# Optimization experiments

Measured on AMD Instinct MI355X. Metric: run time of the kernel, lower is better.

Reference implementation:

```python
import jax, jax.numpy as jnp
import numpy as np

C = 1.2            # PoincareBall curvature (learnable in torch, init value used)
SQC = C ** 0.5
MIN_NORM = 1e-15
BALL_EPS = 4e-3    # geoopt float32 projx eps

def _artanh(x):
    return jnp.arctanh(jnp.clip(x, -1.0 + 1e-7, 1.0 - 1e-7))

def _tanh(x):
    return jnp.tanh(jnp.clip(x, -15.0, 15.0))

def _norm(x):
    return jnp.maximum(jnp.linalg.norm(x, axis=-1, keepdims=True), MIN_NORM)

def p_projx(x):
    n = _norm(x)
    maxnorm = (1.0 - BALL_EPS) / SQC
    return jnp.where(n > maxnorm, x / n * maxnorm, x)

def p_expmap0(u):
    n = _norm(u)
    return p_projx(_tanh(SQC * n) * u / (SQC * n))

def p_logmap0(y):
    n = _norm(y)
    return _artanh(SQC * n) * y / (SQC * n)

def p_mobius_add(x, y):
    x2 = jnp.sum(x * x, -1, keepdims=True)
    y2 = jnp.sum(y * y, -1, keepdims=True)
    xy = jnp.sum(x * y, -1, keepdims=True)
    num = (1 + 2 * C * xy + C * y2) * x + (1 - C * x2) * y
    den = 1 + 2 * C * xy + C * C * x2 * y2
    return num / jnp.maximum(den, MIN_NORM)

def p_mobius_matvec(W, x):
    xn = _norm(x)
    mx = x @ W.T
    mxn = _norm(mx)
    res = _tanh(mxn / xn * _artanh(SQC * xn)) * mx / (mxn * SQC)
    zero = jnp.all(mx == 0, axis=-1, keepdims=True)
    return p_projx(jnp.where(zero, jnp.zeros_like(res), res))

def p_mobius_scalar_mul(r, x):
    n = _norm(x)
    return p_projx(_tanh(r * _artanh(SQC * n)) * x / (n * SQC))

def p_linear(x, W, b):
    # Manifold_Linear on PoincareBall: mobius matvec + mobius bias add + projx
    mv = p_mobius_matvec(W, x)
    return p_projx(p_mobius_add(mv, p_expmap0(b)))

def e_linear(x, W, b):
    return x @ W.T + b

def mob_relu(x):
    # Mob_Act: logmap0 -> act -> expmap0 (with projection)
    return p_expmap0(jax.nn.relu(p_logmap0(x)))


def setup_inputs() -> dict:
    key = jax.random.key(0)
    ks = jax.random.split(key, 26)
    g = lambda i, shape, s: (jax.random.normal(ks[i], shape, jnp.float32) * s)
    d = {
        'x':   g(0, (1024, 32, 128), 1.0),
        'We1': g(1, (80, 32), 0.1),   'be1': g(2, (80,), 0.05),
        'We2': g(3, (104, 80), 0.1),  'be2': g(4, (104,), 0.05),
        'We3': g(5, (128, 104), 0.1), 'be3': g(6, (128,), 0.05),
        'Wh1': g(7, (80, 32), 0.1),   'bh1': g(8, (80,), 0.05),
        'Wh2': g(9, (104, 80), 0.1),  'bh2': g(10, (104,), 0.05),
        'Wh3': g(11, (128, 104), 0.1),'bh3': g(12, (128,), 0.05),
        'Wae': g(13, (128, 128), 0.1),'bae': g(14, (128,), 0.05),
        'Wah': g(15, (128, 128), 0.1),'bah': g(16, (128,), 0.05),
        'Wte': g(17, (1, 128), 0.1),  'bte': g(18, (1,), 0.05),
        'Wth': g(19, (1, 128), 0.1),  'bth': g(20, (1,), 0.05),
        'Wf1': g(21, (10, 256), 0.1), 'bf1': g(22, (10,), 0.05),
        'Wf2': g(23, (10, 10), 0.1),  'bf2': g(24, (10,), 0.05),
    }
    return d


def reference(x, We1, be1, We2, be2, We3, be3,
              Wh1, bh1, Wh2, bh2, Wh3, bh3,
              Wae, bae, Wah, bah, Wte, bte, Wth, bth,
              Wf1, bf1, Wf2, bf2):
    xs = jnp.transpose(x, (0, 2, 1))  # (B, S, C_in)

    # --- Euclidean branch: expmap0 = identity; Manifold_Linear = plain linear ---
    xe = xs
    xe = e_linear(xe, We1, be1); xe = jax.nn.relu(xe)
    xe = e_linear(xe, We2, be2); xe = jax.nn.relu(xe)
    xe = e_linear(xe, We3, be3)
    out_e = jax.nn.relu(xe)               # extra self.act for Euclidean manifolds

    # --- Poincare branch ---
    xh = p_expmap0(xs)
    xh = p_linear(xh, Wh1, bh1); xh = mob_relu(xh)
    xh = p_linear(xh, Wh2, bh2); xh = mob_relu(xh)
    out_h = p_linear(xh, Wh3, bh3)        # (B, S, part_dim)

    # --- cross-manifold attention in tangent space at origin ---
    tan_e = e_linear(out_e, Wae, bae)                    # Euclidean logmap0 = id
    tan_h = p_logmap0(p_linear(out_h, Wah, bah))
    mu = 0.5 * (tan_e + tan_h)
    a_e = e_linear(tan_e - mu, Wte, bte)  # (B, S, 1)
    a_h = e_linear(tan_h - mu, Wth, bth)
    w = jax.nn.softmax(jnp.stack([a_e, a_h], axis=0), axis=0)
    proc_e = w[0] * out_e                                # Euclidean mobius scalar mul
    proc_h = p_mobius_scalar_mul(w[1], out_h)

    # --- pool over constituents in tangent space, concat, classify ---
    o_e = jnp.mean(proc_e, axis=1)                       # Euclidean logmap0 = id
    o_h = jnp.mean(p_logmap0(proc_h), axis=1)
    o = jnp.concatenate([o_e, o_h], axis=-1)             # (B, 2*part_dim)
    o = jax.nn.relu(e_linear(o, Wf1, bf1))
    return e_linear(o, Wf2, bf2)
```

## Files before the change

kernel.cpp:

```cpp
#include <hip/hip_runtime.h>
#include <math.h>

constexpr float CC   = 1.2f;
constexpr float SQC  = 1.09544511501033215f;
constexpr float MAXN = (1.0f - 4e-3f) / SQC;
constexpr float MINN = 1e-15f;

constexpr int WTH1 = 0;
constexpr int WTH2 = 4096;
constexpr int WTH3 = 14336;
constexpr int WTAH = 27648;
constexpr int WTE1 = 44032;
constexpr int WTE2 = 48128;
constexpr int WTE3 = 58368;
constexpr int EB1  = 71680;
constexpr int EB2  = 71808;
constexpr int EB3  = 71936;
constexpr int EBA  = 72064;
constexpr int BE1  = 72192;
constexpr int BE2  = 72320;
constexpr int BE3  = 72448;
constexpr int U1o  = 72576;
constexpr int U2o  = 72704;
constexpr int SCo  = 72832;
constexpr int PART = 72864;

constexpr int ASTR  = 65;
constexpr int L_ACT = 0;
constexpr int L_ZH  = 8320;
constexpr int L_SCR = 8960;
constexpr int L_TOT = 9728;

__device__ __forceinline__ float art_(float x){
  x = fminf(fmaxf(x, -0.9999999f), 0.9999999f);
  return 0.5f * __logf((1.0f + x) / (1.0f - x));
}
__device__ __forceinline__ float tanh_(float x){
  x = fminf(fmaxf(x, -15.0f), 15.0f);
  float e = __expf(2.0f * x);
  return (e - 1.0f) / (e + 1.0f);
}
__device__ __forceinline__ float wsum(float v){
#pragma unroll
  for(int i=32;i>0;i>>=1) v += __shfl_xor(v, i, 64);
  return v;
}
__device__ __forceinline__ float rtj(float v){
  v += __shfl_xor(v, 1, 64); v += __shfl_xor(v, 2, 64);
  v += __shfl_xor(v, 4, 64); v += __shfl_xor(v, 8, 64);
  return v;
}
__device__ __forceinline__ float lamv(float nv){
  float n = fmaxf(nv, MINN);
  return art_(SQC*n)/(SQC*n);
}
struct HS { float ca, cb, nv; };
__device__ __forceinline__ HS hyper_chain(float m2, float meb, float xn_in, float y2){
  float xn  = fmaxf(xn_in, MINN);
  float mxn = fmaxf(sqrtf(m2), MINN);
  float r   = art_(SQC*xn);
  float s   = tanh_(mxn/xn*r)/(mxn*SQC);
  float nr  = s*mxn;
  if(nr > MAXN){ s *= MAXN/nr; nr = MAXN; }
  float xy = s*meb, x2 = nr*nr;
  float den = fmaxf(1.f + 2.f*CC*xy + CC*CC*x2*y2, MINN);
  float A   = (1.f + 2.f*CC*xy + CC*y2)/den;
  float Bc  = (1.f - CC*x2)/den;
  float n3  = sqrtf(fmaxf(A*A*x2 + 2.f*A*Bc*xy + Bc*Bc*y2, 0.f));
  float rho = (n3 > MAXN) ? MAXN/n3 : 1.f;
  HS h; h.nv = fminf(n3, MAXN); h.ca = rho*A*s; h.cb = rho*Bc;
  return h;
}
struct TT { float tau, nf; };
__device__ __forceinline__ TT tail_relu(float rn2){
  float rn = fmaxf(sqrtf(rn2), MINN);
  float th = tanh_(SQC*rn);
  TT r; r.tau = th/(SQC*rn); r.nf = th/SQC;
  if(r.nf > MAXN){ r.tau *= MAXN/r.nf; r.nf = MAXN; }
  return r;
}
struct EX { float nh, scl; };
__device__ __forceinline__ EX exp0(float n2){
  float n0 = fmaxf(sqrtf(n2), MINN);
  float th = tanh_(SQC*n0);
  EX e; e.nh = th/SQC; e.scl = th/(SQC*n0);
  if(e.nh > MAXN){ e.scl *= MAXN/e.nh; e.nh = MAXN; }
  return e;
}
struct THW { float te, th2; };
__device__ __forceinline__ THW ahchain(float m2a, float mw1, float mw2, float meba,
                                       float xnh, float rr, float y2,
                                       float ebw1, float ebw2){
  float mxn = fmaxf(sqrtf(m2a), MINN);
  float s = tanh_(mxn/xnh*rr)/(mxn*SQC);
  float nr = s*mxn;
  if(nr > MAXN){ s *= MAXN/nr; nr = MAXN; }
  float xy = s*meba, x2 = nr*nr;
  float den = fmaxf(1.f + 2.f*CC*xy + CC*CC*x2*y2, MINN);
  float A = (1.f + 2.f*CC*xy + CC*y2)/den;
  float Bc = (1.f - CC*x2)/den;
  float n3 = sqrtf(fmaxf(A*A*x2 + 2.f*A*Bc*xy + Bc*Bc*y2, 0.f));
  float rho = (n3 > MAXN) ? MAXN/n3 : 1.f;
  float nv = fminf(n3, MAXN);
  float lr = lamv(nv)*rho;
  THW r; r.te = lr*(A*s*mw1 + Bc*ebw1); r.th2 = lr*(A*s*mw2 + Bc*ebw2);
  return r;
}
struct AG { float wge, g2; };
__device__ __forceinline__ AG attn(float d1, float d2, float thte, float thth,
                                   float rr, float xnh, float b_e, float b_h){
  float a_e = 0.5f*(d1 - thte) + b_e;
  float a_h = 0.5f*(thth - d2) + b_h;
  float mx = fmaxf(a_e, a_h);
  float ee = __expf(a_e - mx), eh = __expf(a_h - mx);
  float inv = 1.f/(ee + eh);
  AG r; r.wge = ee*inv;
  float wgh = eh*inv;
  float inner = wgh*rr;
  float scl2 = tanh_(inner)/(xnh*SQC);
  float nn = scl2*xnh;
  if(nn > MAXN){ scl2 *= MAXN/nn; nn = MAXN; }
  r.g2 = lamv(nn)*scl2;
  return r;
}

__global__ void k_setup_a(const float* __restrict__ Wae, const float* __restrict__ bae,
                          const float* __restrict__ bh1, const float* __restrict__ bh2,
                          const float* __restrict__ bh3, const float* __restrict__ bah,
                          const float* __restrict__ Wte, const float* __restrict__ Wth,
                          const float* __restrict__ be1, const float* __restrict__ be2,
                          const float* __restrict__ be3, float* __restrict__ ws){
  const int tid = threadIdx.x;
  {
    const int which = tid >> 7, k = tid & 127;
    const float* wv = which ? Wth : Wte;
    float s = 0.f;
#pragma unroll 4
    for(int j=0;j<128;++j) s += Wae[j*128+k] * wv[j];
    ws[(which ? U2o : U1o) + k] = s;
  }
  if(tid < 128){
    ws[BE1+tid] = (tid < 80)  ? be1[tid] : 0.f;
    ws[BE2+tid] = (tid < 104) ? be2[tid] : 0.f;
    ws[BE3+tid] = be3[tid];
  }
  if(tid < 64){
    const int l = tid;
    float p1=0.f, p2=0.f;
    for(int j=l;j<128;j+=64){ p1 += bae[j]*Wte[j]; p2 += bae[j]*Wth[j]; }
    p1 = wsum(p1); p2 = wsum(p2);
    if(l==0){ ws[SCo+0]=p1; ws[SCo+1]=p2; }
    const float* bs[4] = {bh1,bh2,bh3,bah};
    const int dims[4]  = {80,104,128,128};
    const int offs[4]  = {EB1,EB2,EB3,EBA};
    for(int v=0;v<4;++v){
      const float* bp = bs[v]; const int D = dims[v];
      float q = 0.f;
      for(int j=l;j<D;j+=64) q += bp[j]*bp[j];
      q = wsum(q);
      float nb = fmaxf(sqrtf(q), MINN);
      float th = tanhf(fminf(fmaxf(SQC*nb,-15.f),15.f));
      float coef = th/(SQC*nb);
      float ne = th/SQC;
      if(ne > MAXN){ coef *= MAXN/ne; ne = MAXN; }
      for(int j=l;j<D;j+=64) ws[offs[v]+j] = coef*bp[j];
      for(int j=D+l;j<128;j+=64) ws[offs[v]+j] = 0.f;
      if(l==0) ws[SCo+2+v] = ne*ne;
      if(v==3){
        float e1=0.f, e2=0.f;
        for(int j=l;j<D;j+=64){ e1 += bp[j]*Wte[j]; e2 += bp[j]*Wth[j]; }
        e1 = wsum(e1)*coef; e2 = wsum(e2)*coef;
        if(l==0){ ws[SCo+6]=e1; ws[SCo+7]=e2; }
      }
    }
  }
}

__global__ void k_trans(const float* __restrict__ Wh1, const float* __restrict__ Wh2,
                        const float* __restrict__ Wh3, const float* __restrict__ Wah,
                        const float* __restrict__ We1, const float* __restrict__ We2,
                        const float* __restrict__ We3, float* __restrict__ ws){
  const int blk = blockIdx.x, j = threadIdx.x;
  const float* W; int OUT, K, kk, dst;
  if(blk < 32)       { W=Wh1; OUT=80;  K=32;  kk=blk;      dst=WTH1; }
  else if(blk < 112) { W=Wh2; OUT=104; K=80;  kk=blk-32;   dst=WTH2; }
  else if(blk < 216) { W=Wh3; OUT=128; K=104; kk=blk-112;  dst=WTH3; }
  else if(blk < 344) { W=Wah; OUT=128; K=128; kk=blk-216;  dst=WTAH; }
  else if(blk < 376) { W=We1; OUT=80;  K=32;  kk=blk-344;  dst=WTE1; }
  else if(blk < 456) { W=We2; OUT=104; K=80;  kk=blk-376;  dst=WTE2; }
  else               { W=We3; OUT=128; K=104; kk=blk-456;  dst=WTE3; }
  ws[dst + kk*128 + j] = (j < OUT) ? W[j*K + kk] : 0.f;
}

__global__ void k_fin(const float* __restrict__ ws, const float* __restrict__ bf1,
                      const float* __restrict__ Wf2, const float* __restrict__ bf2,
                      float* __restrict__ out){
  const int r = blockIdx.x*64 + threadIdx.x;
  const float* p = ws + PART + (size_t)r*20;
  float f1[10];
#pragma unroll
  for(int i=0;i<10;++i)
    f1[i] = fmaxf((p[i] + p[10+i])*(1.f/128.f) + bf1[i], 0.f);
#pragma unroll
  for(int o=0;o<10;++o){
    float a = bf2[o];
#pragma unroll
    for(int k=0;k<10;++k) a = fmaf(Wf2[o*10+k], f1[k], a);
    out[r*10 + o] = a;
  }
}

__device__ __forceinline__ void ld8(const float* __restrict__ p, float (&v)[8]){
  float4 a = *(const float4*)p, b = *(const float4*)(p+4);
  v[0]=a.x; v[1]=a.y; v[2]=a.z; v[3]=a.w; v[4]=b.x; v[5]=b.y; v[6]=b.z; v[7]=b.w;
}

template<int K, bool XG, bool XSQ>
__device__ __forceinline__ void gemm4(const float* __restrict__ wt,
                                      const float* __restrict__ xg,
                                      const float* __restrict__ ACT,
                                      int tj, int tt, float (&acc)[4][8], float (&xsq)[4]){
#pragma unroll
  for(int i=0;i<4;++i)
#pragma unroll
    for(int j=0;j<8;++j) acc[i][j] = 0.f;
  const int wo = tj*8, xo = tt*4;
#pragma unroll 4
  for(int k=0;k<K;++k){
    float4 w0 = *(const float4*)(wt + k*128 + wo);
    float4 w1 = *(const float4*)(wt + k*128 + wo + 4);
    float4 xa;
    if(XG) xa = *(const float4*)(xg + k*128 + xo);
    else   xa = *(const float4*)(ACT + k*ASTR + xo);
    float xv[4] = {xa.x,xa.y,xa.z,xa.w};
    float wv[8] = {w0.x,w0.y,w0.z,w0.w,w1.x,w1.y,w1.z,w1.w};
#pragma unroll
    for(int i=0;i<4;++i){
      if(XSQ) xsq[i] = fmaf(xv[i], xv[i], xsq[i]);
#pragma unroll
      for(int j=0;j<8;++j) acc[i][j] = fmaf(xv[i], wv[j], acc[i][j]);
    }
  }
}

__device__ __forceinline__ void wACT(float* __restrict__ ACT, const float (&acc)[4][8],
                                     int tj, int tt){
#pragma unroll
  for(int j=0;j<8;++j){
    float4 a = {acc[0][j],acc[1][j],acc[2][j],acc[3][j]};
    *(float4*)(ACT + (tj*8+j)*ASTR + tt*4) = a;
  }
}

__global__ __launch_bounds__(256, 4) void k_main(
    const float* __restrict__ x,
    const float* __restrict__ Wf1, const float* __restrict__ Wte,
    const float* __restrict__ bte, const float* __restrict__ Wth,
    const float* __restrict__ bth, float* __restrict__ ws){
  extern __shared__ float lds[];
  float* ACT = lds + L_ACT;
  float* ZH  = lds + L_ZH;
  float* SCR = lds + L_SCR;
  const int tid = threadIdx.x, tj = tid & 15, tt = tid >> 4;
  const int b = blockIdx.x, b2 = b >> 1, hf = b & 1;
  const int tok0 = tt*4;
  const bool isTok = tid < 64;
  const float* xg = x + (size_t)b2*4096 + hf*64;

  float acc[4][8];
  float xsq[4];
#pragma unroll
  for(int i=0;i<4;++i) xsq[i] = 0.f;

  float nf = 0.f, rr = 0.f, xnh = 1.f, thte = 0.f, thth = 0.f;

  {
    gemm4<32,true,true>(ws+WTH1, xg, ACT, tj, tt, acc, xsq);
    float ebv[8]; ld8(ws+EB1+tj*8, ebv);
#pragma unroll
    for(int i=0;i<4;++i){
      float s=0.f, e=0.f;
#pragma unroll
      for(int j=0;j<8;++j){ s = fmaf(acc[i][j],acc[i][j],s); e = fmaf(acc[i][j],ebv[j],e); }
      s = rtj(s); e = rtj(e);
      if(tj==0){ SCR[tok0+i]=s; SCR[64+tok0+i]=e; SCR[128+tok0+i]=xsq[i]; }
    }
    __syncthreads();
    if(isTok){
      EX e0 = exp0(SCR[128+tid]);
      float scl0 = e0.scl;
      float m2 = SCR[tid]*scl0*scl0, meb = SCR[64+tid]*scl0;
      HS h = hyper_chain(m2, meb, e0.nh, ws[SCo+2]);
      SCR[tid] = h.ca*scl0; SCR[64+tid] = h.cb; SCR[128+tid] = lamv(h.nv);
    }
    __syncthreads();
    float cav[4],cbv[4],lmv[4];
#pragma unroll
    for(int i=0;i<4;++i){ cav[i]=SCR[tok0+i]; cbv[i]=SCR[64+tok0+i]; lmv[i]=SCR[128+tok0+i]; }
#pragma unroll
    for(int i=0;i<4;++i){
      float s=0.f;
#pragma unroll
      for(int j=0;j<8;++j){
        float v = fmaxf(lmv[i]*fmaf(cav[i],acc[i][j],cbv[i]*ebv[j]), 0.f);
        acc[i][j]=v; s = fmaf(v,v,s);
      }
      s = rtj(s);
      if(tj==0) SCR[192+tok0+i]=s;
    }
    __syncthreads();
    if(isTok){ TT tr = tail_relu(SCR[192+tid]); nf = tr.nf; SCR[192+tid]=tr.tau; }
    __syncthreads();
#pragma unroll
    for(int i=0;i<4;++i){ float tau=SCR[192+tok0+i];
#pragma unroll
      for(int j=0;j<8;++j) acc[i][j]*=tau; }
    wACT(ACT, acc, tj, tt);
    __syncthreads();
  }

  {
    gemm4<80,false,false>(ws+WTH2, nullptr, ACT, tj, tt, acc, xsq);
    float ebv[8]; ld8(ws+EB2+tj*8, ebv);
#pragma unroll
    for(int i=0;i<4;++i){
      float s=0.f, e=0.f;
#pragma unroll
      for(int j=0;j<8;++j){ s = fmaf(acc[i][j],acc[i][j],s); e = fmaf(acc[i][j],ebv[j],e); }
      s = rtj(s); e = rtj(e);
      if(tj==0){ SCR[tok0+i]=s; SCR[64+tok0+i]=e; }
    }
    __syncthreads();
    if(isTok){
      HS h = hyper_chain(SCR[tid], SCR[64+tid], nf, ws[SCo+3]);
      SCR[tid]=h.ca; SCR[64+tid]=h.cb; SCR[128+tid]=lamv(h.nv);
    }
    __syncthreads();
    float cav[4],cbv[4],lmv[4];
#pragma unroll
    for(int i=0;i<4;++i){ cav[i]=SCR[tok0+i]; cbv[i]=SCR[64+tok0+i]; lmv[i]=SCR[128+tok0+i]; }
#pragma unroll
    for(int i=0;i<4;++i){
      float s=0.f;
#pragma unroll
      for(int j=0;j<8;++j){
        float v = fmaxf(lmv[i]*fmaf(cav[i],acc[i][j],cbv[i]*ebv[j]), 0.f);
        acc[i][j]=v; s = fmaf(v,v,s);
      }
      s = rtj(s);
      if(tj==0) SCR[192+tok0+i]=s;
    }
    __syncthreads();
    if(isTok){ TT tr = tail_relu(SCR[192+tid]); nf = tr.nf; SCR[192+tid]=tr.tau; }
    __syncthreads();
#pragma unroll
    for(int i=0;i<4;++i){ float tau=SCR[192+tok0+i];
#pragma unroll
      for(int j=0;j<8;++j) acc[i][j]*=tau; }
    wACT(ACT, acc, tj, tt);
    __syncthreads();
  }

  {
    gemm4<104,false,false>(ws+WTH3, nullptr, ACT, tj, tt, acc, xsq);
    float ebv[8]; ld8(ws+EB3+tj*8, ebv);
#pragma unroll
    for(int i=0;i<4;++i){
      float s=0.f, e=0.f;
#pragma unroll
      for(int j=0;j<8;++j){ s = fmaf(acc[i][j],acc[i][j],s); e = fmaf(acc[i][j],ebv[j],e); }
      s = rtj(s); e = rtj(e);
      if(tj==0){ SCR[tok0+i]=s; SCR[64+tok0+i]=e; }
    }
    __syncthreads();
    if(isTok){
      HS h = hyper_chain(SCR[tid], SCR[64+tid], nf, ws[SCo+4]);
      xnh = fmaxf(h.nv, MINN);
      rr  = art_(SQC*xnh);
      SCR[tid]=h.ca; SCR[64+tid]=h.cb;
    }
    __syncthreads();
    float cav[4],cbv[4];
#pragma unroll
    for(int i=0;i<4;++i){ cav[i]=SCR[tok0+i]; cbv[i]=SCR[64+tok0+i]; }
#pragma unroll
    for(int i=0;i<4;++i)
#pragma unroll
      for(int j=0;j<8;++j) acc[i][j] = fmaf(cav[i],acc[i][j],cbv[i]*ebv[j]);
    wACT(ACT, acc, tj, tt);
#pragma unroll
    for(int ic=0;ic<10;++ic){
      float wf[8]; ld8(Wf1 + ic*256 + 128 + tj*8, wf);
#pragma unroll
      for(int i=0;i<4;++i){
        float s=0.f;
#pragma unroll
        for(int j=0;j<8;++j) s = fmaf(acc[i][j], wf[j], s);
        s = rtj(s);
        if(tj==0) ZH[ic*64 + tok0 + i] = s;
      }
    }
    __syncthreads();
  }

  {
    gemm4<128,false,false>(ws+WTAH, nullptr, ACT, tj, tt, acc, xsq);
    float w1v[8], w2v[8], eav[8];
    ld8(Wte + tj*8, w1v); ld8(Wth + tj*8, w2v); ld8(ws+EBA+tj*8, eav);
#pragma unroll
    for(int i=0;i<4;++i){
      float s0=0.f,s1=0.f,s2=0.f,s3=0.f;
#pragma unroll
      for(int j=0;j<8;++j){
        float m = acc[i][j];
        s0 = fmaf(m,m,s0); s1 = fmaf(m,w1v[j],s1);
        s2 = fmaf(m,w2v[j],s2); s3 = fmaf(m,eav[j],s3);
      }
      s0=rtj(s0); s1=rtj(s1); s2=rtj(s2); s3=rtj(s3);
      if(tj==0){ SCR[tok0+i]=s0; SCR[64+tok0+i]=s1; SCR[128+tok0+i]=s2; SCR[192+tok0+i]=s3; }
    }
    __syncthreads();
    if(isTok){
      THW a = ahchain(SCR[tid], SCR[64+tid], SCR[128+tid], SCR[192+tid],
                      xnh, rr, ws[SCo+5], ws[SCo+6], ws[SCo+7]);
      thte = a.te; thth = a.th2;
    }
  }

  {
    gemm4<32,true,false>(ws+WTE1, xg, ACT, tj, tt, acc, xsq);
    float bev[8]; ld8(ws+BE1+tj*8, bev);
#pragma unroll
    for(int i=0;i<4;++i)
#pragma unroll
      for(int j=0;j<8;++j) acc[i][j] = fmaxf(acc[i][j]+bev[j], 0.f);
    __syncthreads();
    wACT(ACT, acc, tj, tt);
    __syncthreads();
  }
  {
    gemm4<80,false,false>(ws+WTE2, nullptr, ACT, tj, tt, acc, xsq);
    float bev[8]; ld8(ws+BE2+tj*8, bev);
#pragma unroll
    for(int i=0;i<4;++i)
#pragma unroll
      for(int j=0;j<8;++j) acc[i][j] = fmaxf(acc[i][j]+bev[j], 0.f);
    __syncthreads();
    wACT(ACT, acc, tj, tt);
    __syncthreads();
  }
  {
    gemm4<104,false,false>(ws+WTE3, nullptr, ACT, tj, tt, acc, xsq);
    float bev[8], u1v[8], u2v[8];
    ld8(ws+BE3+tj*8, bev); ld8(ws+U1o+tj*8, u1v); ld8(ws+U2o+tj*8, u2v);
#pragma unroll
    for(int i=0;i<4;++i){
      float s1=0.f, s2=0.f;
#pragma unroll
      for(int j=0;j<8;++j){
        float v = fmaxf(acc[i][j]+bev[j], 0.f);
        acc[i][j] = v;
        s1 = fmaf(v,u1v[j],s1); s2 = fmaf(v,u2v[j],s2);
      }
      s1=rtj(s1); s2=rtj(s2);
      if(tj==0){ SCR[tok0+i]=s1; SCR[64+tok0+i]=s2; }
    }
#pragma unroll
    for(int ic=0;ic<10;++ic){
      float wf[8]; ld8(Wf1 + ic*256 + tj*8, wf);
#pragma unroll
      for(int i=0;i<4;++i){
        float s=0.f;
#pragma unroll
        for(int j=0;j<8;++j) s = fmaf(acc[i][j], wf[j], s);
        s = rtj(s);
        if(tj==0) SCR[(2+ic)*64 + tok0 + i] = s;
      }
    }
    __syncthreads();
    if(isTok){
      float d1 = SCR[tid] + ws[SCo+0];
      float d2 = SCR[64+tid] + ws[SCo+1];
      AG g = attn(d1, d2, thte, thth, rr, xnh, bte[0], bth[0]);
      float pv[10];
#pragma unroll
      for(int ic=0;ic<10;++ic){
        float p = fmaf(g.wge, SCR[(2+ic)*64+tid], g.g2 * ZH[ic*64+tid]);
        pv[ic] = wsum(p);
      }
      if(tid == 0){
#pragma unroll
        for(int ic=0;ic<10;++ic) ws[PART + (size_t)b*10 + ic] = pv[ic];
      }
    }
  }
}

extern "C" void kernel_launch(void* const* d_in, const int* in_sizes, int n_in,
                              void* d_out, int out_size, void* d_ws, size_t ws_size,
                              hipStream_t stream){
  (void)in_sizes; (void)n_in; (void)out_size; (void)ws_size;
  const float* x   = (const float*)d_in[0];
  const float* We1 = (const float*)d_in[1];
  const float* be1 = (const float*)d_in[2];
  const float* We2 = (const float*)d_in[3];
  const float* be2 = (const float*)d_in[4];
  const float* We3 = (const float*)d_in[5];
  const float* be3 = (const float*)d_in[6];
  const float* Wh1 = (const float*)d_in[7];
  const float* bh1 = (const float*)d_in[8];
  const float* Wh2 = (const float*)d_in[9];
  const float* bh2 = (const float*)d_in[10];
  const float* Wh3 = (const float*)d_in[11];
  const float* bh3 = (const float*)d_in[12];
  const float* Wae = (const float*)d_in[13];
  const float* bae = (const float*)d_in[14];
  const float* Wah = (const float*)d_in[15];
  const float* bah = (const float*)d_in[16];
  const float* Wte = (const float*)d_in[17];
  const float* bte = (const float*)d_in[18];
  const float* Wth = (const float*)d_in[19];
  const float* bth = (const float*)d_in[20];
  const float* Wf1 = (const float*)d_in[21];
  const float* bf1 = (const float*)d_in[22];
  const float* Wf2 = (const float*)d_in[23];
  const float* bf2 = (const float*)d_in[24];
  float* ws  = (float*)d_ws;
  float* out = (float*)d_out;

  hipLaunchKernelGGL(k_setup_a, dim3(1), dim3(256), 0, stream,
                     Wae, bae, bh1, bh2, bh3, bah, Wte, Wth, be1, be2, be3, ws);
  hipLaunchKernelGGL(k_trans, dim3(560), dim3(128), 0, stream,
                     Wh1, Wh2, Wh3, Wah, We1, We2, We3, ws);

  const int smem = L_TOT * 4;
  hipLaunchKernelGGL(k_main, dim3(2048), dim3(256), smem, stream,
                     x, Wf1, Wte, bte, Wth, bth, ws);

  hipLaunchKernelGGL(k_fin, dim3(16), dim3(64), 0, stream,
                     ws, bf1, Wf2, bf2, out);
}
```

Baseline: 568.6 us.

## Compute per-token hyperbolic scalars redundantly in every lane, removing block barriers

Per-token scalar chains (hyper_chain, tail_relu, ahchain, attn) were computed by 64 threads through LDS staging with several __syncthreads per layer. They are now computed redundantly in each of the 16 lanes that hold a token, right after the row reductions, so most barriers and LDS round-trips go away. The final pooling reduces with shuffles plus a small cross-wave LDS sum, and the setup and transpose kernels are merged into one launch. LDS allocation shrinks, which may help occupancy. In exchange, all lanes repeat the transcendental math and register pressure rises from the per-token arrays.

```diff
diff --git a/kernel.cpp b/kernel.cpp
--- a/kernel.cpp
+++ b/kernel.cpp
@@ -29,7 +29,7 @@
 constexpr int L_ACT = 0;
 constexpr int L_ZH  = 8320;
 constexpr int L_SCR = 8960;
-constexpr int L_TOT = 9728;
+constexpr int L_TOT = 9000;
 
 __device__ __forceinline__ float art_(float x){
   x = fminf(fmaxf(x, -0.9999999f), 0.9999999f);
@@ -124,13 +124,31 @@
   return r;
 }
 
-__global__ void k_setup_a(const float* __restrict__ Wae, const float* __restrict__ bae,
-                          const float* __restrict__ bh1, const float* __restrict__ bh2,
-                          const float* __restrict__ bh3, const float* __restrict__ bah,
-                          const float* __restrict__ Wte, const float* __restrict__ Wth,
-                          const float* __restrict__ be1, const float* __restrict__ be2,
-                          const float* __restrict__ be3, float* __restrict__ ws){
-  const int tid = threadIdx.x;
+__global__ void k_setup(const float* __restrict__ Wh1, const float* __restrict__ Wh2,
+                        const float* __restrict__ Wh3, const float* __restrict__ Wah,
+                        const float* __restrict__ We1, const float* __restrict__ We2,
+                        const float* __restrict__ We3,
+                        const float* __restrict__ Wae, const float* __restrict__ bae,
+                        const float* __restrict__ bh1, const float* __restrict__ bh2,
+                        const float* __restrict__ bh3, const float* __restrict__ bah,
+                        const float* __restrict__ Wte, const float* __restrict__ Wth,
+                        const float* __restrict__ be1, const float* __restrict__ be2,
+                        const float* __restrict__ be3, float* __restrict__ ws){
+  const int blk = blockIdx.x, tid = threadIdx.x;
+  if(blk < 280){
+    const int row = blk*2 + (tid >> 7);
+    const int j   = tid & 127;
+    const float* W; int OUT, K, kk, dst;
+    if(row < 32)       { W=Wh1; OUT=80;  K=32;  kk=row;      dst=WTH1; }
+    else if(row < 112) { W=Wh2; OUT=104; K=80;  kk=row-32;   dst=WTH2; }
+    else if(row < 216) { W=Wh3; OUT=128; K=104; kk=row-112;  dst=WTH3; }
+    else if(row < 344) { W=Wah; OUT=128; K=128; kk=row-216;  dst=WTAH; }
+    else if(row < 376) { W=We1; OUT=80;  K=32;  kk=row-344;  dst=WTE1; }
+    else if(row < 456) { W=We2; OUT=104; K=80;  kk=row-376;  dst=WTE2; }
+    else               { W=We3; OUT=128; K=104; kk=row-456;  dst=WTE3; }
+    ws[dst + kk*128 + j] = (j < OUT) ? W[j*K + kk] : 0.f;
+    return;
+  }
   {
     const int which = tid >> 7, k = tid & 127;
     const float* wv = which ? Wth : Wte;
@@ -176,22 +194,6 @@
   }
 }
 
-__global__ void k_trans(const float* __restrict__ Wh1, const float* __restrict__ Wh2,
-                        const float* __restrict__ Wh3, const float* __restrict__ Wah,
-                        const float* __restrict__ We1, const float* __restrict__ We2,
-                        const float* __restrict__ We3, float* __restrict__ ws){
-  const int blk = blockIdx.x, j = threadIdx.x;
-  const float* W; int OUT, K, kk, dst;
-  if(blk < 32)       { W=Wh1; OUT=80;  K=32;  kk=blk;      dst=WTH1; }
-  else if(blk < 112) { W=Wh2; OUT=104; K=80;  kk=blk-32;   dst=WTH2; }
-  else if(blk < 216) { W=Wh3; OUT=128; K=104; kk=blk-112;  dst=WTH3; }
-  else if(blk < 344) { W=Wah; OUT=128; K=128; kk=blk-216;  dst=WTAH; }
-  else if(blk < 376) { W=We1; OUT=80;  K=32;  kk=blk-344;  dst=WTE1; }
-  else if(blk < 456) { W=We2; OUT=104; K=80;  kk=blk-376;  dst=WTE2; }
-  else               { W=We3; OUT=128; K=104; kk=blk-456;  dst=WTE3; }
-  ws[dst + kk*128 + j] = (j < OUT) ? W[j*K + kk] : 0.f;
-}
-
 __global__ void k_fin(const float* __restrict__ ws, const float* __restrict__ bf1,
                       const float* __restrict__ Wf2, const float* __restrict__ bf2,
                       float* __restrict__ out){
@@ -264,15 +266,19 @@
   const int tid = threadIdx.x, tj = tid & 15, tt = tid >> 4;
   const int b = blockIdx.x, b2 = b >> 1, hf = b & 1;
   const int tok0 = tt*4;
-  const bool isTok = tid < 64;
   const float* xg = x + (size_t)b2*4096 + hf*64;
+
+  const float c1  = ws[SCo+0], c2  = ws[SCo+1];
+  const float y21 = ws[SCo+2], y22 = ws[SCo+3], y23 = ws[SCo+4], y2a = ws[SCo+5];
+  const float ew1 = ws[SCo+6], ew2 = ws[SCo+7];
+  const float btev = bte[0], bthv = bth[0];
 
   float acc[4][8];
   float xsq[4];
 #pragma unroll
   for(int i=0;i<4;++i) xsq[i] = 0.f;
 
-  float nf = 0.f, rr = 0.f, xnh = 1.f, thte = 0.f, thth = 0.f;
+  float nf[4], xnh[4], rr[4], tte[4], tth[4];
 
   {
     gemm4<32,true,true>(ws+WTH1, xg, ACT, tj, tt, acc, xsq);
@@ -283,38 +289,20 @@
 #pragma unroll
       for(int j=0;j<8;++j){ s = fmaf(acc[i][j],acc[i][j],s); e = fmaf(acc[i][j],ebv[j],e); }
       s = rtj(s); e = rtj(e);
-      if(tj==0){ SCR[tok0+i]=s; SCR[64+tok0+i]=e; SCR[128+tok0+i]=xsq[i]; }
-    }
-    __syncthreads();
-    if(isTok){
-      EX e0 = exp0(SCR[128+tid]);
-      float scl0 = e0.scl;
-      float m2 = SCR[tid]*scl0*scl0, meb = SCR[64+tid]*scl0;
-      HS h = hyper_chain(m2, meb, e0.nh, ws[SCo+2]);
-      SCR[tid] = h.ca*scl0; SCR[64+tid] = h.cb; SCR[128+tid] = lamv(h.nv);
-    }
-    __syncthreads();
-    float cav[4],cbv[4],lmv[4];
-#pragma unroll
-    for(int i=0;i<4;++i){ cav[i]=SCR[tok0+i]; cbv[i]=SCR[64+tok0+i]; lmv[i]=SCR[128+tok0+i]; }
-#pragma unroll
-    for(int i=0;i<4;++i){
-      float s=0.f;
+      EX e0 = exp0(xsq[i]);
+      HS h = hyper_chain(s*e0.scl*e0.scl, e*e0.scl, e0.nh, y21);
+      float lam = lamv(h.nv), ca = h.ca*e0.scl, cb = h.cb;
+      float s2 = 0.f;
 #pragma unroll
       for(int j=0;j<8;++j){
-        float v = fmaxf(lmv[i]*fmaf(cav[i],acc[i][j],cbv[i]*ebv[j]), 0.f);
-        acc[i][j]=v; s = fmaf(v,v,s);
-      }
-      s = rtj(s);
-      if(tj==0) SCR[192+tok0+i]=s;
-    }
-    __syncthreads();
-    if(isTok){ TT tr = tail_relu(SCR[192+tid]); nf = tr.nf; SCR[192+tid]=tr.tau; }
-    __syncthreads();
-#pragma unroll
-    for(int i=0;i<4;++i){ float tau=SCR[192+tok0+i];
-#pragma unroll
-      for(int j=0;j<8;++j) acc[i][j]*=tau; }
+        float v = fmaxf(lam*fmaf(ca, acc[i][j], cb*ebv[j]), 0.f);
+        acc[i][j] = v; s2 = fmaf(v,v,s2);
+      }
+      s2 = rtj(s2);
+      TT tr = tail_relu(s2); nf[i] = tr.nf;
+#pragma unroll
+      for(int j=0;j<8;++j) acc[i][j] *= tr.tau;
+    }
     wACT(ACT, acc, tj, tt);
     __syncthreads();
   }
@@ -328,35 +316,20 @@
 #pragma unroll
       for(int j=0;j<8;++j){ s = fmaf(acc[i][j],acc[i][j],s); e = fmaf(acc[i][j],ebv[j],e); }
       s = rtj(s); e = rtj(e);
-      if(tj==0){ SCR[tok0+i]=s; SCR[64+tok0+i]=e; }
-    }
-    __syncthreads();
-    if(isTok){
-      HS h = hyper_chain(SCR[tid], SCR[64+tid], nf, ws[SCo+3]);
-      SCR[tid]=h.ca; SCR[64+tid]=h.cb; SCR[128+tid]=lamv(h.nv);
-    }
-    __syncthreads();
-    float cav[4],cbv[4],lmv[4];
-#pragma unroll
-    for(int i=0;i<4;++i){ cav[i]=SCR[tok0+i]; cbv[i]=SCR[64+tok0+i]; lmv[i]=SCR[128+tok0+i]; }
-#pragma unroll
-    for(int i=0;i<4;++i){
-      float s=0.f;
+      HS h = hyper_chain(s, e, nf[i], y22);
+      float lam = lamv(h.nv);
+      float s2 = 0.f;
 #pragma unroll
       for(int j=0;j<8;++j){
-        float v = fmaxf(lmv[i]*fmaf(cav[i],acc[i][j],cbv[i]*ebv[j]), 0.f);
-        acc[i][j]=v; s = fmaf(v,v,s);
-      }
-      s = rtj(s);
-      if(tj==0) SCR[192+tok0+i]=s;
-    }
-    __syncthreads();
-    if(isTok){ TT tr = tail_relu(SCR[192+tid]); nf = tr.nf; SCR[192+tid]=tr.tau; }
-    __syncthreads();
-#pragma unroll
-    for(int i=0;i<4;++i){ float tau=SCR[192+tok0+i];
-#pragma unroll
-      for(int j=0;j<8;++j) acc[i][j]*=tau; }
+        float v = fmaxf(lam*fmaf(h.ca, acc[i][j], h.cb*ebv[j]), 0.f);
+        acc[i][j] = v; s2 = fmaf(v,v,s2);
+      }
+      s2 = rtj(s2);
+      TT tr = tail_relu(s2); nf[i] = tr.nf;
+#pragma unroll
+      for(int j=0;j<8;++j) acc[i][j] *= tr.tau;
+    }
+    __syncthreads();
     wACT(ACT, acc, tj, tt);
     __syncthreads();
   }
@@ -370,23 +343,13 @@
 #pragma unroll
       for(int j=0;j<8;++j){ s = fmaf(acc[i][j],acc[i][j],s); e = fmaf(acc[i][j],ebv[j],e); }
       s = rtj(s); e = rtj(e);
-      if(tj==0){ SCR[tok0+i]=s; SCR[64+tok0+i]=e; }
-    }
-    __syncthreads();
-    if(isTok){
-      HS h = hyper_chain(SCR[tid], SCR[64+tid], nf, ws[SCo+4]);
-      xnh = fmaxf(h.nv, MINN);
-      rr  = art_(SQC*xnh);
-      SCR[tid]=h.ca; SCR[64+tid]=h.cb;
-    }
-    __syncthreads();
-    float cav[4],cbv[4];
-#pragma unroll
-    for(int i=0;i<4;++i){ cav[i]=SCR[tok0+i]; cbv[i]=SCR[64+tok0+i]; }
-#pragma unroll
-    for(int i=0;i<4;++i)
-#pragma unroll
-      for(int j=0;j<8;++j) acc[i][j] = fmaf(cav[i],acc[i][j],cbv[i]*ebv[j]);
+      HS h = hyper_chain(s, e, nf[i], y23);
+      xnh[i] = fmaxf(h.nv, MINN);
+      rr[i]  = art_(SQC*xnh[i]);
+#pragma unroll
+      for(int j=0;j<8;++j) acc[i][j] = fmaf(h.ca, acc[i][j], h.cb*ebv[j]);
+    }
+    __syncthreads();
     wACT(ACT, acc, tj, tt);
 #pragma unroll
     for(int ic=0;ic<10;++ic){
@@ -417,13 +380,8 @@
         s2 = fmaf(m,w2v[j],s2); s3 = fmaf(m,eav[j],s3);
       }
       s0=rtj(s0); s1=rtj(s1); s2=rtj(s2); s3=rtj(s3);
-      if(tj==0){ SCR[tok0+i]=s0; SCR[64+tok0+i]=s1; SCR[128+tok0+i]=s2; SCR[192+tok0+i]=s3; }
-    }
-    __syncthreads();
-    if(isTok){
-      THW a = ahchain(SCR[tid], SCR[64+tid], SCR[128+tid], SCR[192+tid],
-                      xnh, rr, ws[SCo+5], ws[SCo+6], ws[SCo+7]);
-      thte = a.te; thth = a.th2;
+      THW a = ahchain(s0, s1, s2, s3, xnh[i], rr[i], y2a, ew1, ew2);
+      tte[i] = a.te; tth[i] = a.th2;
     }
   }
 
@@ -453,6 +411,7 @@
     gemm4<104,false,false>(ws+WTE3, nullptr, ACT, tj, tt, acc, xsq);
     float bev[8], u1v[8], u2v[8];
     ld8(ws+BE3+tj*8, bev); ld8(ws+U1o+tj*8, u1v); ld8(ws+U2o+tj*8, u2v);
+    float wge[4], g2v[4];
 #pragma unroll
     for(int i=0;i<4;++i){
       float s1=0.f, s2=0.f;
@@ -462,37 +421,30 @@
         acc[i][j] = v;
         s1 = fmaf(v,u1v[j],s1); s2 = fmaf(v,u2v[j],s2);
       }
-      s1=rtj(s1); s2=rtj(s2);
-      if(tj==0){ SCR[tok0+i]=s1; SCR[64+tok0+i]=s2; }
+      s1 = rtj(s1); s2 = rtj(s2);
+      AG g = attn(s1 + c1, s2 + c2, tte[i], tth[i], rr[i], xnh[i], btev, bthv);
+      wge[i] = g.wge; g2v[i] = g.g2;
     }
 #pragma unroll
     for(int ic=0;ic<10;++ic){
       float wf[8]; ld8(Wf1 + ic*256 + tj*8, wf);
+      float pv = 0.f;
 #pragma unroll
       for(int i=0;i<4;++i){
-        float s=0.f;
-#pragma unroll
-        for(int j=0;j<8;++j) s = fmaf(acc[i][j], wf[j], s);
-        s = rtj(s);
-        if(tj==0) SCR[(2+ic)*64 + tok0 + i] = s;
-      }
-    }
-    __syncthreads();
-    if(isTok){
-      float d1 = SCR[tid] + ws[SCo+0];
-      float d2 = SCR[64+tid] + ws[SCo+1];
-      AG g = attn(d1, d2, thte, thth, rr, xnh, bte[0], bth[0]);
-      float pv[10];
-#pragma unroll
-      for(int ic=0;ic<10;++ic){
-        float p = fmaf(g.wge, SCR[(2+ic)*64+tid], g.g2 * ZH[ic*64+tid]);
-        pv[ic] = wsum(p);
-      }
-      if(tid == 0){
-#pragma unroll
-        for(int ic=0;ic<10;++ic) ws[PART + (size_t)b*10 + ic] = pv[ic];
-      }
-    }
+        float z=0.f;
+#pragma unroll
+        for(int j=0;j<8;++j) z = fmaf(acc[i][j], wf[j], z);
+        z = rtj(z);
+        pv += wge[i]*z + g2v[i]*ZH[ic*64 + tok0 + i];
+      }
+      pv += __shfl_xor(pv, 16, 64);
+      pv += __shfl_xor(pv, 32, 64);
+      if((tid & 63) == 0) SCR[(tid>>6)*10 + ic] = pv;
+    }
+    __syncthreads();
+    if(tid < 10)
+      ws[PART + (size_t)b*10 + tid] =
+        SCR[tid] + SCR[10+tid] + SCR[20+tid] + SCR[30+tid];
   }
 }
 
@@ -528,10 +480,9 @@
   float* ws  = (float*)d_ws;
   float* out = (float*)d_out;
 
-  hipLaunchKernelGGL(k_setup_a, dim3(1), dim3(256), 0, stream,
+  hipLaunchKernelGGL(k_setup, dim3(281), dim3(256), 0, stream,
+                     Wh1, Wh2, Wh3, Wah, We1, We2, We3,
                      Wae, bae, bh1, bh2, bh3, bah, Wte, Wth, be1, be2, be3, ws);
-  hipLaunchKernelGGL(k_trans, dim3(560), dim3(128), 0, stream,
-                     Wh1, Wh2, Wh3, Wah, We1, We2, We3, ws);
 
   const int smem = L_TOT * 4;
   hipLaunchKernelGGL(k_main, dim3(2048), dim3(256), smem, stream,
```

Result: slower. 590.8 us (+3.9%).

## Split each sample across four blocks of 32 tokens and merge setup kernels

Applied to the files above, without the earlier changes.

The main kernel now processes 32 tokens per block instead of 64. The grid doubles to 4096 blocks, the register tile shrinks to 2x8, LDS use drops by about half, and launch bounds rise to 6 blocks per CU to raise occupancy. The final kernel now sums four partials per sample instead of two. The weight-transpose and setup kernels are fused into one launch, and extra barriers are added before the activation writes. In exchange each block reloads the full weights for half as many tokens, so weight traffic per token rises and arithmetic reuse drops.

```diff
diff --git a/kernel.cpp b/kernel.cpp
--- a/kernel.cpp
+++ b/kernel.cpp
@@ -25,11 +25,11 @@
 constexpr int SCo  = 72832;
 constexpr int PART = 72864;
 
-constexpr int ASTR  = 65;
+constexpr int ASTR  = 33;
 constexpr int L_ACT = 0;
-constexpr int L_ZH  = 8320;
-constexpr int L_SCR = 8960;
-constexpr int L_TOT = 9728;
+constexpr int L_ZH  = 4224;
+constexpr int L_SCR = 4544;
+constexpr int L_TOT = 4928;
 
 __device__ __forceinline__ float art_(float x){
   x = fminf(fmaxf(x, -0.9999999f), 0.9999999f);
@@ -48,6 +48,12 @@
 __device__ __forceinline__ float rtj(float v){
   v += __shfl_xor(v, 1, 64); v += __shfl_xor(v, 2, 64);
   v += __shfl_xor(v, 4, 64); v += __shfl_xor(v, 8, 64);
+  return v;
+}
+__device__ __forceinline__ float rt32(float v){
+  v += __shfl_xor(v, 1, 64); v += __shfl_xor(v, 2, 64);
+  v += __shfl_xor(v, 4, 64); v += __shfl_xor(v, 8, 64);
+  v += __shfl_xor(v, 16, 64);
   return v;
 }
 __device__ __forceinline__ float lamv(float nv){
@@ -124,13 +130,31 @@
   return r;
 }
 
-__global__ void k_setup_a(const float* __restrict__ Wae, const float* __restrict__ bae,
-                          const float* __restrict__ bh1, const float* __restrict__ bh2,
-                          const float* __restrict__ bh3, const float* __restrict__ bah,
-                          const float* __restrict__ Wte, const float* __restrict__ Wth,
-                          const float* __restrict__ be1, const float* __restrict__ be2,
-                          const float* __restrict__ be3, float* __restrict__ ws){
-  const int tid = threadIdx.x;
+__global__ void k_setup(const float* __restrict__ Wh1, const float* __restrict__ Wh2,
+                        const float* __restrict__ Wh3, const float* __restrict__ Wah,
+                        const float* __restrict__ We1, const float* __restrict__ We2,
+                        const float* __restrict__ We3,
+                        const float* __restrict__ Wae, const float* __restrict__ bae,
+                        const float* __restrict__ bh1, const float* __restrict__ bh2,
+                        const float* __restrict__ bh3, const float* __restrict__ bah,
+                        const float* __restrict__ Wte, const float* __restrict__ Wth,
+                        const float* __restrict__ be1, const float* __restrict__ be2,
+                        const float* __restrict__ be3, float* __restrict__ ws){
+  const int blk = blockIdx.x, tid = threadIdx.x;
+  if(blk < 280){
+    const int row = blk*2 + (tid >> 7);
+    const int j   = tid & 127;
+    const float* W; int OUT, K, kk, dst;
+    if(row < 32)       { W=Wh1; OUT=80;  K=32;  kk=row;      dst=WTH1; }
+    else if(row < 112) { W=Wh2; OUT=104; K=80;  kk=row-32;   dst=WTH2; }
+    else if(row < 216) { W=Wh3; OUT=128; K=104; kk=row-112;  dst=WTH3; }
+    else if(row < 344) { W=Wah; OUT=128; K=128; kk=row-216;  dst=WTAH; }
+    else if(row < 376) { W=We1; OUT=80;  K=32;  kk=row-344;  dst=WTE1; }
+    else if(row < 456) { W=We2; OUT=104; K=80;  kk=row-376;  dst=WTE2; }
+    else               { W=We3; OUT=128; K=104; kk=row-456;  dst=WTE3; }
+    ws[dst + kk*128 + j] = (j < OUT) ? W[j*K + kk] : 0.f;
+    return;
+  }
   {
     const int which = tid >> 7, k = tid & 127;
     const float* wv = which ? Wth : Wte;
@@ -176,31 +200,15 @@
   }
 }
 
-__global__ void k_trans(const float* __restrict__ Wh1, const float* __restrict__ Wh2,
-                        const float* __restrict__ Wh3, const float* __restrict__ Wah,
-                        const float* __restrict__ We1, const float* __restrict__ We2,
-                        const float* __restrict__ We3, float* __restrict__ ws){
-  const int blk = blockIdx.x, j = threadIdx.x;
-  const float* W; int OUT, K, kk, dst;
-  if(blk < 32)       { W=Wh1; OUT=80;  K=32;  kk=blk;      dst=WTH1; }
-  else if(blk < 112) { W=Wh2; OUT=104; K=80;  kk=blk-32;   dst=WTH2; }
-  else if(blk < 216) { W=Wh3; OUT=128; K=104; kk=blk-112;  dst=WTH3; }
-  else if(blk < 344) { W=Wah; OUT=128; K=128; kk=blk-216;  dst=WTAH; }
-  else if(blk < 376) { W=We1; OUT=80;  K=32;  kk=blk-344;  dst=WTE1; }
-  else if(blk < 456) { W=We2; OUT=104; K=80;  kk=blk-376;  dst=WTE2; }
-  else               { W=We3; OUT=128; K=104; kk=blk-456;  dst=WTE3; }
-  ws[dst + kk*128 + j] = (j < OUT) ? W[j*K + kk] : 0.f;
-}
-
 __global__ void k_fin(const float* __restrict__ ws, const float* __restrict__ bf1,
                       const float* __restrict__ Wf2, const float* __restrict__ bf2,
                       float* __restrict__ out){
   const int r = blockIdx.x*64 + threadIdx.x;
-  const float* p = ws + PART + (size_t)r*20;
+  const float* p = ws + PART + (size_t)r*40;
   float f1[10];
 #pragma unroll
   for(int i=0;i<10;++i)
-    f1[i] = fmaxf((p[i] + p[10+i])*(1.f/128.f) + bf1[i], 0.f);
+    f1[i] = fmaxf((p[i] + p[10+i] + p[20+i] + p[30+i])*(1.f/128.f) + bf1[i], 0.f);
 #pragma unroll
   for(int o=0;o<10;++o){
     float a = bf2[o];
@@ -216,26 +224,26 @@
 }
 
 template<int K, bool XG, bool XSQ>
-__device__ __forceinline__ void gemm4(const float* __restrict__ wt,
+__device__ __forceinline__ void gemm2(const float* __restrict__ wt,
                                       const float* __restrict__ xg,
                                       const float* __restrict__ ACT,
-                                      int tj, int tt, float (&acc)[4][8], float (&xsq)[4]){
-#pragma unroll
-  for(int i=0;i<4;++i)
+                                      int tj, int tt, float (&acc)[2][8], float (&xsq)[2]){
+#pragma unroll
+  for(int i=0;i<2;++i)
 #pragma unroll
     for(int j=0;j<8;++j) acc[i][j] = 0.f;
-  const int wo = tj*8, xo = tt*4;
+  const int wo = tj*8, xo = tt*2;
 #pragma unroll 4
   for(int k=0;k<K;++k){
     float4 w0 = *(const float4*)(wt + k*128 + wo);
     float4 w1 = *(const float4*)(wt + k*128 + wo + 4);
-    float4 xa;
-    if(XG) xa = *(const float4*)(xg + k*128 + xo);
-    else   xa = *(const float4*)(ACT + k*ASTR + xo);
-    float xv[4] = {xa.x,xa.y,xa.z,xa.w};
+    float2 xa;
+    if(XG) xa = *(const float2*)(xg + k*128 + xo);
+    else   xa = *(const float2*)(ACT + k*ASTR + xo);
+    float xv[2] = {xa.x,xa.y};
     float wv[8] = {w0.x,w0.y,w0.z,w0.w,w1.x,w1.y,w1.z,w1.w};
 #pragma unroll
-    for(int i=0;i<4;++i){
+    for(int i=0;i<2;++i){
       if(XSQ) xsq[i] = fmaf(xv[i], xv[i], xsq[i]);
 #pragma unroll
       for(int j=0;j<8;++j) acc[i][j] = fmaf(xv[i], wv[j], acc[i][j]);
@@ -243,16 +251,16 @@
   }
 }
 
-__device__ __forceinline__ void wACT(float* __restrict__ ACT, const float (&acc)[4][8],
+__device__ __forceinline__ void wACT(float* __restrict__ ACT, const float (&acc)[2][8],
                                      int tj, int tt){
 #pragma unroll
   for(int j=0;j<8;++j){
-    float4 a = {acc[0][j],acc[1][j],acc[2][j],acc[3][j]};
-    *(float4*)(ACT + (tj*8+j)*ASTR + tt*4) = a;
-  }
-}
-
-__global__ __launch_bounds__(256, 4) void k_main(
+    float2 a = {acc[0][j],acc[1][j]};
+    *(float2*)(ACT + (tj*8+j)*ASTR + tt*2) = a;
+  }
+}
+
+__global__ __launch_bounds__(256, 6) void k_main(
     const float* __restrict__ x,
     const float* __restrict__ Wf1, const float* __restrict__ Wte,
     const float* __restrict__ bte, const float* __restrict__ Wth,
@@ -262,43 +270,43 @@
   float* ZH  = lds + L_ZH;
   float* SCR = lds + L_SCR;
   const int tid = threadIdx.x, tj = tid & 15, tt = tid >> 4;
-  const int b = blockIdx.x, b2 = b >> 1, hf = b & 1;
-  const int tok0 = tt*4;
-  const bool isTok = tid < 64;
-  const float* xg = x + (size_t)b2*4096 + hf*64;
-
-  float acc[4][8];
-  float xsq[4];
-#pragma unroll
-  for(int i=0;i<4;++i) xsq[i] = 0.f;
+  const int b = blockIdx.x, b2 = b >> 2, q = b & 3;
+  const int tok0 = tt*2;
+  const bool isTok = tid < 32;
+  const float* xg = x + (size_t)b2*4096 + q*32;
+
+  float acc[2][8];
+  float xsq[2];
+#pragma unroll
+  for(int i=0;i<2;++i) xsq[i] = 0.f;
 
   float nf = 0.f, rr = 0.f, xnh = 1.f, thte = 0.f, thth = 0.f;
 
   {
-    gemm4<32,true,true>(ws+WTH1, xg, ACT, tj, tt, acc, xsq);
+    gemm2<32,true,true>(ws+WTH1, xg, ACT, tj, tt, acc, xsq);
     float ebv[8]; ld8(ws+EB1+tj*8, ebv);
 #pragma unroll
-    for(int i=0;i<4;++i){
+    for(int i=0;i<2;++i){
       float s=0.f, e=0.f;
 #pragma unroll
       for(int j=0;j<8;++j){ s = fmaf(acc[i][j],acc[i][j],s); e = fmaf(acc[i][j],ebv[j],e); }
       s = rtj(s); e = rtj(e);
-      if(tj==0){ SCR[tok0+i]=s; SCR[64+tok0+i]=e; SCR[128+tok0+i]=xsq[i]; }
+      if(tj==0){ SCR[tok0+i]=s; SCR[32+tok0+i]=e; SCR[64+tok0+i]=xsq[i]; }
     }
     __syncthreads();
     if(isTok){
-      EX e0 = exp0(SCR[128+tid]);
+      EX e0 = exp0(SCR[64+tid]);
       float scl0 = e0.scl;
-      float m2 = SCR[tid]*scl0*scl0, meb = SCR[64+tid]*scl0;
+      float m2 = SCR[tid]*scl0*scl0, meb = SCR[32+tid]*scl0;
       HS h = hyper_chain(m2, meb, e0.nh, ws[SCo+2]);
-      SCR[tid] = h.ca*scl0; SCR[64+tid] = h.cb; SCR[128+tid] = lamv(h.nv);
-    }
-    __syncthreads();
-    float cav[4],cbv[4],lmv[4];
-#pragma unroll
-    for(int i=0;i<4;++i){ cav[i]=SCR[tok0+i]; cbv[i]=SCR[64+tok0+i]; lmv[i]=SCR[128+tok0+i]; }
-#pragma unroll
-    for(int i=0;i<4;++i){
+      SCR[tid] = h.ca*scl0; SCR[32+tid] = h.cb; SCR[64+tid] = lamv(h.nv);
+    }
+    __syncthreads();
+    float cav[2],cbv[2],lmv[2];
+#pragma unroll
+    for(int i=0;i<2;++i){ cav[i]=SCR[tok0+i]; cbv[i]=SCR[32+tok0+i]; lmv[i]=SCR[64+tok0+i]; }
+#pragma unroll
+    for(int i=0;i<2;++i){
       float s=0.f;
 #pragma unroll
       for(int j=0;j<8;++j){
@@ -306,13 +314,13 @@
         acc[i][j]=v; s = fmaf(v,v,s);
       }
       s = rtj(s);
-      if(tj==0) SCR[192+tok0+i]=s;
-    }
-    __syncthreads();
-    if(isTok){ TT tr = tail_relu(SCR[192+tid]); nf = tr.nf; SCR[192+tid]=tr.tau; }
-    __syncthreads();
-#pragma unroll
-    for(int i=0;i<4;++i){ float tau=SCR[192+tok0+i];
+      if(tj==0) SCR[96+tok0+i]=s;
+    }
+    __syncthreads();
+    if(isTok){ TT tr = tail_relu(SCR[96+tid]); nf = tr.nf; SCR[96+tid]=tr.tau; }
+    __syncthreads();
+#pragma unroll
+    for(int i=0;i<2;++i){ float tau=SCR[96+tok0+i];
 #pragma unroll
       for(int j=0;j<8;++j) acc[i][j]*=tau; }
     wACT(ACT, acc, tj, tt);
@@ -320,27 +328,27 @@
   }
 
   {
-    gemm4<80,false,false>(ws+WTH2, nullptr, ACT, tj, tt, acc, xsq);
+    gemm2<80,false,false>(ws+WTH2, nullptr, ACT, tj, tt, acc, xsq);
     float ebv[8]; ld8(ws+EB2+tj*8, ebv);
 #pragma unroll
-    for(int i=0;i<4;++i){
+    for(int i=0;i<2;++i){
       float s=0.f, e=0.f;
 #pragma unroll
       for(int j=0;j<8;++j){ s = fmaf(acc[i][j],acc[i][j],s); e = fmaf(acc[i][j],ebv[j],e); }
       s = rtj(s); e = rtj(e);
-      if(tj==0){ SCR[tok0+i]=s; SCR[64+tok0+i]=e; }
+      if(tj==0){ SCR[tok0+i]=s; SCR[32+tok0+i]=e; }
     }
     __syncthreads();
     if(isTok){
-      HS h = hyper_chain(SCR[tid], SCR[64+tid], nf, ws[SCo+3]);
-      SCR[tid]=h.ca; SCR[64+tid]=h.cb; SCR[128+tid]=lamv(h.nv);
-    }
-    __syncthreads();
-    float cav[4],cbv[4],lmv[4];
-#pragma unroll
-    for(int i=0;i<4;++i){ cav[i]=SCR[tok0+i]; cbv[i]=SCR[64+tok0+i]; lmv[i]=SCR[128+tok0+i]; }
-#pragma unroll
-    for(int i=0;i<4;++i){
+      HS h = hyper_chain(SCR[tid], SCR[32+tid], nf, ws[SCo+3]);
+      SCR[tid]=h.ca; SCR[32+tid]=h.cb; SCR[64+tid]=lamv(h.nv);
+    }
+    __syncthreads();
+    float cav[2],cbv[2],lmv[2];
+#pragma unroll
+    for(int i=0;i<2;++i){ cav[i]=SCR[tok0+i]; cbv[i]=SCR[32+tok0+i]; lmv[i]=SCR[64+tok0+i]; }
+#pragma unroll
+    for(int i=0;i<2;++i){
       float s=0.f;
 #pragma unroll
       for(int j=0;j<8;++j){
@@ -348,67 +356,69 @@
         acc[i][j]=v; s = fmaf(v,v,s);
       }
       s = rtj(s);
-      if(tj==0) SCR[192+tok0+i]=s;
-    }
-    __syncthreads();
-    if(isTok){ TT tr = tail_relu(SCR[192+tid]); nf = tr.nf; SCR[192+tid]=tr.tau; }
-    __syncthreads();
-#pragma unroll
-    for(int i=0;i<4;++i){ float tau=SCR[192+tok0+i];
+      if(tj==0) SCR[96+tok0+i]=s;
+    }
+    __syncthreads();
+    if(isTok){ TT tr = tail_relu(SCR[96+tid]); nf = tr.nf; SCR[96+tid]=tr.tau; }
+    __syncthreads();
+#pragma unroll
+    for(int i=0;i<2;++i){ float tau=SCR[96+tok0+i];
 #pragma unroll
       for(int j=0;j<8;++j) acc[i][j]*=tau; }
+    __syncthreads();
     wACT(ACT, acc, tj, tt);
     __syncthreads();
   }
 
   {
-    gemm4<104,false,false>(ws+WTH3, nullptr, ACT, tj, tt, acc, xsq);
+    gemm2<104,false,false>(ws+WTH3, nullptr, ACT, tj, tt, acc, xsq);
     float ebv[8]; ld8(ws+EB3+tj*8, ebv);
 #pragma unroll
-    for(int i=0;i<4;++i){
+    for(int i=0;i<2;++i){
       float s=0.f, e=0.f;
 #pragma unroll
       for(int j=0;j<8;++j){ s = fmaf(acc[i][j],acc[i][j],s); e = fmaf(acc[i][j],ebv[j],e); }
       s = rtj(s); e = rtj(e);
-      if(tj==0){ SCR[tok0+i]=s; SCR[64+tok0+i]=e; }
+      if(tj==0){ SCR[tok0+i]=s; SCR[32+tok0+i]=e; }
     }
     __syncthreads();
     if(isTok){
-      HS h = hyper_chain(SCR[tid], SCR[64+tid], nf, ws[SCo+4]);
+      HS h = hyper_chain(SCR[tid], SCR[32+tid], nf, ws[SCo+4]);
       xnh = fmaxf(h.nv, MINN);
       rr  = art_(SQC*xnh);
-      SCR[tid]=h.ca; SCR[64+tid]=h.cb;
-    }
-    __syncthreads();
-    float cav[4],cbv[4];
-#pragma unroll
-    for(int i=0;i<4;++i){ cav[i]=SCR[tok0+i]; cbv[i]=SCR[64+tok0+i]; }
-#pragma unroll
-    for(int i=0;i<4;++i)
+      SCR[tid]=h.ca; SCR[32+tid]=h.cb;
+    }
+    __syncthreads();
+    float cav[2],cbv[2];
+#pragma unroll
+    for(int i=0;i<2;++i){ cav[i]=SCR[tok0+i]; cbv[i]=SCR[32+tok0+i]; }
+#pragma unroll
+    for(int i=0;i<2;++i)
 #pragma unroll
       for(int j=0;j<8;++j) acc[i][j] = fmaf(cav[i],acc[i][j],cbv[i]*ebv[j]);
+    __syncthreads();
     wACT(ACT, acc, tj, tt);
 #pragma unroll
     for(int ic=0;ic<10;++ic){
       float wf[8]; ld8(Wf1 + ic*256 + 128 + tj*8, wf);
 #pragma unroll
-      for(int i=0;i<4;++i){
+      for(int i=0;i<2;++i){
         float s=0.f;
 #pragma unroll
         for(int j=0;j<8;++j) s = fmaf(acc[i][j], wf[j], s);
         s = rtj(s);
-        if(tj==0) ZH[ic*64 + tok0 + i] = s;
-      }
-    }
-    __syncthreads();
-  }
-
-  {
-    gemm4<128,false,false>(ws+WTAH, nullptr, ACT, tj, tt, acc, xsq);
+        if(tj==0) ZH[ic*32 + tok0 + i] = s;
+      }
+    }
+    __syncthreads();
+  }
+
+  {
+    gemm2<128,false,false>(ws+WTAH, nullptr, ACT, tj, tt, acc, xsq);
     float w1v[8], w2v[8], eav[8];
     ld8(Wte + tj*8, w1v); ld8(Wth + tj*8, w2v); ld8(ws+EBA+tj*8, eav);
 #pragma unroll
-    for(int i=0;i<4;++i){
+    for(int i=0;i<2;++i){
       float s0=0.f,s1=0.f,s2=0.f,s3=0.f;
 #pragma unroll
       for(int j=0;j<8;++j){
@@ -417,21 +427,21 @@
         s2 = fmaf(m,w2v[j],s2); s3 = fmaf(m,eav[j],s3);
       }
       s0=rtj(s0); s1=rtj(s1); s2=rtj(s2); s3=rtj(s3);
-      if(tj==0){ SCR[tok0+i]=s0; SCR[64+tok0+i]=s1; SCR[128+tok0+i]=s2; SCR[192+tok0+i]=s3; }
+      if(tj==0){ SCR[tok0+i]=s0; SCR[32+tok0+i]=s1; SCR[64+tok0+i]=s2; SCR[96+tok0+i]=s3; }
     }
     __syncthreads();
     if(isTok){
-      THW a = ahchain(SCR[tid], SCR[64+tid], SCR[128+tid], SCR[192+tid],
+      THW a = ahchain(SCR[tid], SCR[32+tid], SCR[64+tid], SCR[96+tid],
                       xnh, rr, ws[SCo+5], ws[SCo+6], ws[SCo+7]);
       thte = a.te; thth = a.th2;
     }
   }
 
   {
-    gemm4<32,true,false>(ws+WTE1, xg, ACT, tj, tt, acc, xsq);
+    gemm2<32,true,false>(ws+WTE1, xg, ACT, tj, tt, acc, xsq);
     float bev[8]; ld8(ws+BE1+tj*8, bev);
 #pragma unroll
-    for(int i=0;i<4;++i)
+    for(int i=0;i<2;++i)
 #pragma unroll
       for(int j=0;j<8;++j) acc[i][j] = fmaxf(acc[i][j]+bev[j], 0.f);
     __syncthreads();
@@ -439,10 +449,10 @@
     __syncthreads();
   }
   {
-    gemm4<80,false,false>(ws+WTE2, nullptr, ACT, tj, tt, acc, xsq);
+    gemm2<80,false,false>(ws+WTE2, nullptr, ACT, tj, tt, acc, xsq);
     float bev[8]; ld8(ws+BE2+tj*8, bev);
 #pragma unroll
-    for(int i=0;i<4;++i)
+    for(int i=0;i<2;++i)
 #pragma unroll
       for(int j=0;j<8;++j) acc[i][j] = fmaxf(acc[i][j]+bev[j], 0.f);
     __syncthreads();
@@ -450,11 +460,11 @@
     __syncthreads();
   }
   {
-    gemm4<104,false,false>(ws+WTE3, nullptr, ACT, tj, tt, acc, xsq);
+    gemm2<104,false,false>(ws+WTE3, nullptr, ACT, tj, tt, acc, xsq);
     float bev[8], u1v[8], u2v[8];
     ld8(ws+BE3+tj*8, bev); ld8(ws+U1o+tj*8, u1v); ld8(ws+U2o+tj*8, u2v);
 #pragma unroll
-    for(int i=0;i<4;++i){
+    for(int i=0;i<2;++i){
       float s1=0.f, s2=0.f;
 #pragma unroll
       for(int j=0;j<8;++j){
@@ -463,30 +473,30 @@
         s1 = fmaf(v,u1v[j],s1); s2 = fmaf(v,u2v[j],s2);
       }
       s1=rtj(s1); s2=rtj(s2);
-      if(tj==0){ SCR[tok0+i]=s1; SCR[64+tok0+i]=s2; }
+      if(tj==0){ SCR[tok0+i]=s1; SCR[32+tok0+i]=s2; }
     }
 #pragma unroll
     for(int ic=0;ic<10;++ic){
       float wf[8]; ld8(Wf1 + ic*256 + tj*8, wf);
 #pragma unroll
-      for(int i=0;i<4;++i){
+      for(int i=0;i<2;++i){
         float s=0.f;
 #pragma unroll
         for(int j=0;j<8;++j) s = fmaf(acc[i][j], wf[j], s);
         s = rtj(s);
-        if(tj==0) SCR[(2+ic)*64 + tok0 + i] = s;
+        if(tj==0) SCR[(2+ic)*32 + tok0 + i] = s;
       }
     }
     __syncthreads();
     if(isTok){
       float d1 = SCR[tid] + ws[SCo+0];
-      float d2 = SCR[64+tid] + ws[SCo+1];
+      float d2 = SCR[32+tid] + ws[SCo+1];
       AG g = attn(d1, d2, thte, thth, rr, xnh, bte[0], bth[0]);
       float pv[10];
 #pragma unroll
       for(int ic=0;ic<10;++ic){
-        float p = fmaf(g.wge, SCR[(2+ic)*64+tid], g.g2 * ZH[ic*64+tid]);
-        pv[ic] = wsum(p);
+        float p = fmaf(g.wge, SCR[(2+ic)*32+tid], g.g2 * ZH[ic*32+tid]);
+        pv[ic] = rt32(p);
       }
       if(tid == 0){
 #pragma unroll
@@ -528,13 +538,12 @@
   float* ws  = (float*)d_ws;
   float* out = (float*)d_out;
 
-  hipLaunchKernelGGL(k_setup_a, dim3(1), dim3(256), 0, stream,
+  hipLaunchKernelGGL(k_setup, dim3(281), dim3(256), 0, stream,
+                     Wh1, Wh2, Wh3, Wah, We1, We2, We3,
                      Wae, bae, bh1, bh2, bh3, bah, Wte, Wth, be1, be2, be3, ws);
-  hipLaunchKernelGGL(k_trans, dim3(560), dim3(128), 0, stream,
-                     Wh1, Wh2, Wh3, Wah, We1, We2, We3, ws);
 
   const int smem = L_TOT * 4;
-  hipLaunchKernelGGL(k_main, dim3(2048), dim3(256), smem, stream,
+  hipLaunchKernelGGL(k_main, dim3(4096), dim3(256), smem, stream,
                      x, Wf1, Wte, bte, Wth, bth, ws);
 
   hipLaunchKernelGGL(k_fin, dim3(16), dim3(64), 0, stream,
```

Result: slower. 718.3 us (+26.3%).
